# Kernel tuning notes

Measured on AMD Instinct MI355X. Metric: run time of the kernel, lower is better.

## Reference

```python
import jax, jax.numpy as jnp
import numpy as np

B, L, D_IN, D_MODEL, D_STATE, N_LAYERS = 16, 2048, 64, 512, 16, 4
LN_EPS = 1e-5


def setup_inputs() -> dict:
    key = jax.random.key(0)
    ks = jax.random.split(key, 16)
    s = 0.02
    x = jax.random.normal(ks[0], (B, L, D_IN), jnp.float32)
    W_in0 = jax.random.normal(ks[1], (D_IN, D_MODEL), jnp.float32) * s
    b_in0 = jnp.zeros((D_MODEL,), jnp.float32)
    W_in = jax.random.normal(ks[2], (N_LAYERS - 1, D_MODEL, D_MODEL), jnp.float32) * s
    b_in = jnp.zeros((N_LAYERS - 1, D_MODEL), jnp.float32)
    # S4D-style init: A_log = log(1..N) per channel
    A_log = jnp.broadcast_to(jnp.log(jnp.arange(1, D_STATE + 1, dtype=jnp.float32)), (N_LAYERS, D_MODEL, D_STATE)).copy()
    D_skip = jnp.ones((N_LAYERS, D_MODEL), jnp.float32)
    W_dt = jax.random.normal(ks[3], (N_LAYERS, D_MODEL, D_MODEL), jnp.float32) * s
    b_dt = jnp.full((N_LAYERS, D_MODEL), -4.0, jnp.float32)  # small initial dt
    W_B = jax.random.normal(ks[4], (N_LAYERS, D_MODEL, D_STATE), jnp.float32) * s
    W_C = jax.random.normal(ks[5], (N_LAYERS, D_MODEL, D_STATE), jnp.float32) * s
    ln_g = jnp.ones((D_MODEL,), jnp.float32)
    ln_b = jnp.zeros((D_MODEL,), jnp.float32)
    head_w = jax.random.normal(ks[6], (D_MODEL, 1), jnp.float32) * s
    head_b = jnp.zeros((1,), jnp.float32)
    return {"x": x, "W_in0": W_in0, "b_in0": b_in0, "W_in": W_in, "b_in": b_in,
            "A_log": A_log, "D_skip": D_skip, "W_dt": W_dt, "b_dt": b_dt,
            "W_B": W_B, "W_C": W_C, "ln_g": ln_g, "ln_b": ln_b,
            "head_w": head_w, "head_b": head_b}


def _mamba_layer(x, W_in_l, b_in_l, A_log_l, D_l, W_dt_l, b_dt_l, W_B_l, W_C_l):
    # x: (B, L, d_in) -> y: (B, L, D_MODEL)
    u = x @ W_in_l + b_in_l                    # (B, L, D)
    dt = jax.nn.softplus(u @ W_dt_l + b_dt_l)  # (B, L, D)
    Bm = u @ W_B_l                             # (B, L, N)
    Cm = u @ W_C_l                             # (B, L, N)
    A = -jnp.exp(A_log_l)                      # (D, N)

    def step(h, inp):
        dt_t, u_t, B_t, C_t = inp              # (B,D),(B,D),(B,N),(B,N)
        dA = jnp.exp(dt_t[..., None] * A)      # (B, D, N)
        h = dA * h + (dt_t * u_t)[..., None] * B_t[:, None, :]
        y_t = jnp.einsum('bdn,bn->bd', h, C_t)
        return h, y_t

    h0 = jnp.zeros((u.shape[0], u.shape[2], A.shape[1]), u.dtype)
    xs = (jnp.swapaxes(dt, 0, 1), jnp.swapaxes(u, 0, 1),
          jnp.swapaxes(Bm, 0, 1), jnp.swapaxes(Cm, 0, 1))
    _, ys = jax.lax.scan(step, h0, xs)         # ys: (L, B, D)
    return jnp.swapaxes(ys, 0, 1) + u * D_l


def reference(x, W_in0, b_in0, W_in, b_in, A_log, D_skip, W_dt, b_dt, W_B, W_C, ln_g, ln_b, head_w, head_b):
    h = x
    for i in range(N_LAYERS):
        Wi = W_in0 if i == 0 else W_in[i - 1]
        bi = b_in0 if i == 0 else b_in[i - 1]
        h = _mamba_layer(h, Wi, bi, A_log[i], D_skip[i], W_dt[i], b_dt[i], W_B[i], W_C[i])
    # LayerNorm over d_model
    mu = jnp.mean(h, axis=-1, keepdims=True)
    var = jnp.mean(jnp.square(h - mu), axis=-1, keepdims=True)
    h = (h - mu) * jax.lax.rsqrt(var + LN_EPS) * ln_g + ln_b
    return h[:, -1, :] @ head_w + head_b       # (B, 1)
```

## Files before the change

### kernel.cpp

```cpp
#include <hip/hip_runtime.h>
#include <hip/hip_bf16.h>
#include <cstdint>
#include <cstddef>

#define B_SZ    16
#define L_SZ    2048
#define DIN     64
#define DMODEL  512
#define DSTATE  16
#define NLAYERS 4
#define LN_EPS  1e-5f
#define NC      32
#define TCH     (L_SZ / NC)
#define NFUSED  (2 * DMODEL)

typedef __bf16 bf16x8 __attribute__((ext_vector_type(8)));
typedef float  f32x4  __attribute__((ext_vector_type(4)));
typedef unsigned short u16;
typedef unsigned int   u32;

__device__ __forceinline__ u16 f2bf(float f) {
    u32 u = __builtin_bit_cast(u32, f);
    u += 0x7fffu + ((u >> 16) & 1u);
    return (u16)(u >> 16);
}
__device__ __forceinline__ float bf2f(u16 v) {
    u32 u = ((u32)v) << 16;
    return __builtin_bit_cast(float, u);
}

__device__ __forceinline__ void pow16(float q, float* a_) {
    float q2 = q * q, q4 = q2 * q2, q8 = q4 * q4;
    a_[0] = q;        a_[1] = q2;       a_[2] = q2 * q;   a_[3] = q4;
    a_[4] = q4 * q;   a_[5] = q4 * q2;  a_[6] = a_[5] * q; a_[7] = q8;
    a_[8] = q8 * q;   a_[9] = q8 * q2;  a_[10] = a_[9] * q; a_[11] = q8 * q4;
    a_[12] = a_[11] * q; a_[13] = a_[11] * q2; a_[14] = a_[13] * q; a_[15] = q8 * q8;
}

#define LOG2E 1.4426950408889634f

__device__ __forceinline__ void gload16(const void* g, void* l) {
    __builtin_amdgcn_global_load_lds(
        (__attribute__((address_space(1))) void*)(g),
        (__attribute__((address_space(3))) void*)(l), 16, 0, 0);
}

template <int K>
__global__ __launch_bounds__(512) void gemm_fused(
    const u16* __restrict__ A, const u16* __restrict__ BT,
    const float* __restrict__ bias, u16* __restrict__ Cu,
    u16* __restrict__ Cdt, int M)
{
    constexpr int BM = 128, BK = 64;
    constexpr int NT = K / BK;
    __shared__ u16 As[2][BM * BK];
    __shared__ u16 Bs[2][BM * BK];

    const int tid = threadIdx.x;
    const int wv = tid >> 6, ln = tid & 63;
    const int mb = blockIdx.x & 255, nb = blockIdx.x >> 8;
    const int bm = mb * BM, bn = nb * BM;
    const int wm = (wv >> 1) * 32, wn = (wv & 1) * 64;

    f32x4 acc[2][4];
#pragma unroll
    for (int i = 0; i < 2; ++i)
#pragma unroll
        for (int j = 0; j < 4; ++j) acc[i][j] = (f32x4){0.f, 0.f, 0.f, 0.f};

    auto stage = [&](int buf, int k0) {
#pragma unroll
        for (int i = 0; i < 2; ++i) {
            int t = i * 512 + tid;
            int m = t >> 3, s = t & 7;
            int ksrc = (s ^ (m & 7)) * 8;
            gload16(A + (size_t)(bm + m) * K + k0 + ksrc,
                    &As[buf][(i * 512 + wv * 64) * 8]);
            gload16(BT + (size_t)(bn + m) * K + k0 + ksrc,
                    &Bs[buf][(i * 512 + wv * 64) * 8]);
        }
    };

    stage(0, 0);
    if (NT > 1) stage(1, BK);

#pragma unroll
    for (int kt = 0; kt < NT; ++kt) {
        if (kt == NT - 1) asm volatile("s_waitcnt vmcnt(0)" ::: "memory");
        else              asm volatile("s_waitcnt vmcnt(4)" ::: "memory");
        __builtin_amdgcn_s_barrier();

        const int buf = kt & 1;
#pragma unroll
        for (int ks = 0; ks < 2; ++ks) {
            bf16x8 af[2], bfr[4];
            const int g = ln >> 4, lm = ln & 15;
            const int c = ks * 4 + g;
#pragma unroll
            for (int e = 0; e < 2; ++e) {
                int ml = wm + e * 16 + lm;
                af[e] = *(const bf16x8*)&As[buf][ml * 64 + ((c ^ (ml & 7)) * 8)];
            }
#pragma unroll
            for (int f = 0; f < 4; ++f) {
                int nl = wn + f * 16 + lm;
                bfr[f] = *(const bf16x8*)&Bs[buf][nl * 64 + ((c ^ (nl & 7)) * 8)];
            }
#pragma unroll
            for (int e = 0; e < 2; ++e)
#pragma unroll
                for (int f = 0; f < 4; ++f)
                    acc[e][f] = __builtin_amdgcn_mfma_f32_16x16x32_bf16(
                        af[e], bfr[f], acc[e][f], 0, 0, 0);
        }

        asm volatile("s_waitcnt lgkmcnt(0)" ::: "memory");
        __builtin_amdgcn_s_barrier();
        if (kt + 2 < NT) stage(buf, (kt + 2) * BK);
    }

    const int cg = ln >> 4, lc = ln & 15;
    const bool uside = (bn < DMODEL);
#pragma unroll
    for (int e = 0; e < 2; ++e) {
#pragma unroll
        for (int f = 0; f < 4; ++f) {
            int col = bn + wn + f * 16 + lc;
            float bv = bias[col];
#pragma unroll
            for (int r = 0; r < 4; ++r) {
                int row = bm + wm + e * 16 + cg * 4 + r;
                float v = acc[e][f][r] + bv;
                if (uside) {
                    Cu[(size_t)row * DMODEL + col] = f2bf(v);
                } else {
                    v = (v > 20.f) ? v : __logf(1.f + __expf(v));
                    Cdt[(size_t)row * DMODEL + (col - DMODEL)] = f2bf(v);
                }
            }
        }
    }
}

__global__ __launch_bounds__(256) void wtrans(
    const float* __restrict__ W, u16* __restrict__ WT, int K, int N,
    size_t inStride, size_t outStride)
{
    __shared__ float tile[32][33];
    const float* Wm = W + (size_t)blockIdx.z * inStride;
    u16* WTm = WT + (size_t)blockIdx.z * outStride;
    int k0 = blockIdx.x * 32, n0 = blockIdx.y * 32;
    int tx = threadIdx.x & 31, ty = threadIdx.x >> 5;
#pragma unroll
    for (int i = 0; i < 4; ++i)
        tile[ty + 8 * i][tx] = Wm[(size_t)(k0 + ty + 8 * i) * N + n0 + tx];
    __syncthreads();
#pragma unroll
    for (int i = 0; i < 4; ++i)
        WTm[(size_t)(n0 + ty + 8 * i) * K + k0 + tx] = f2bf(tile[tx][ty + 8 * i]);
}

__global__ __launch_bounds__(256) void wcombo(
    const float* __restrict__ Win, const float* __restrict__ Wdt,
    u16* __restrict__ outT, int KD,
    size_t winStride, size_t wdtStride, size_t outStride)
{
    __shared__ float wi[16][516];
    __shared__ float wd[512][16];
    const float* WinL = Win + (size_t)blockIdx.z * winStride;
    const float* WdtL = Wdt + (size_t)blockIdx.z * wdtStride;
    u16* outL = outT + (size_t)blockIdx.z * outStride;
    const int k0 = blockIdx.x * 16, n0 = blockIdx.y * 16;
    const int tid = threadIdx.x;
    for (int i = tid; i < 16 * 128; i += 256) {
        int r = i >> 7, c = i & 127;
        *(float4*)&wi[r][c * 4] =
            *(const float4*)&WinL[(size_t)(k0 + r) * DMODEL + c * 4];
    }
    for (int i = tid; i < 512 * 4; i += 256) {
        int j = i >> 2, c = i & 3;
        *(float4*)&wd[j][c * 4] =
            *(const float4*)&WdtL[(size_t)j * DMODEL + n0 + c * 4];
    }
    __syncthreads();
    const int kk = tid & 15, nn = tid >> 4;
    float acc = 0.f;
#pragma unroll 8
    for (int j = 0; j < 512; ++j)
        acc = fmaf(wi[kk][j], wd[j][nn], acc);
    outL[(size_t)(n0 + nn) * KD + k0 + kk] = f2bf(acc);
}

__global__ __launch_bounds__(256) void biasprep(
    const float* __restrict__ bin, const float* __restrict__ Wdt,
    const float* __restrict__ bdt, float* __restrict__ biascat,
    size_t binStride, size_t wdtStride, size_t bdtStride, size_t outStride)
{
    const float* binL = bin + (size_t)blockIdx.z * binStride;
    const float* WdtL = Wdt + (size_t)blockIdx.z * wdtStride;
    const float* bdtL = bdt + (size_t)blockIdx.z * bdtStride;
    float* outL = biascat + (size_t)blockIdx.z * outStride;
    int idx = blockIdx.x * 256 + threadIdx.x;
    if (idx < DMODEL) { outL[idx] = binL[idx]; return; }
    int n = idx - DMODEL;
    float acc = bdtL[n];
    for (int j = 0; j < DMODEL; ++j)
        acc = fmaf(binL[j], WdtL[(size_t)j * DMODEL + n], acc);
    outL[idx] = acc;
}

__global__ __launch_bounds__(256) void castx(
    const float* __restrict__ x, u16* __restrict__ xb, int n4)
{
    int i = blockIdx.x * 256 + threadIdx.x;
    if (i < n4) {
        float4 v = ((const float4*)x)[i];
        ushort4 o;
        o.x = f2bf(v.x); o.y = f2bf(v.y); o.z = f2bf(v.z); o.w = f2bf(v.w);
        ((ushort4*)xb)[i] = o;
    }
}

__global__ __launch_bounds__(256) void prep_wbc(
    const float* __restrict__ WB, const float* __restrict__ WC,
    u16* __restrict__ WBCT)
{
    int idx = blockIdx.x * 256 + threadIdx.x;
    int l = idx >> 14;
    int r = idx & 16383;
    int n = r >> 9, k = r & 511;
    float v = (n < 16) ? WB[((size_t)l * DMODEL + k) * DSTATE + n]
                       : WC[((size_t)l * DMODEL + k) * DSTATE + (n - 16)];
    WBCT[((size_t)l * 32 + n) * DMODEL + k] = f2bf(v);
}

__global__ __launch_bounds__(256) void gemm_bc_mfma(
    const u16* __restrict__ A, const u16* __restrict__ WBCT,
    float* __restrict__ Bo, float* __restrict__ Co)
{
    const int tid = threadIdx.x;
    const int wv = tid >> 6, ln = tid & 63;
    const int m0 = blockIdx.x * 64 + wv * 16;
    const int g = ln >> 4, lm = ln & 15;

    f32x4 accB = (f32x4){0.f, 0.f, 0.f, 0.f};
    f32x4 accC = (f32x4){0.f, 0.f, 0.f, 0.f};
    const u16* arow = A + (size_t)(m0 + lm) * DMODEL;
    const u16* wb = WBCT + (size_t)lm * DMODEL;
    const u16* wc = WBCT + (size_t)(lm + 16) * DMODEL;
#pragma unroll
    for (int ks = 0; ks < DMODEL / 32; ++ks) {
        int ko = ks * 32 + g * 8;
        bf16x8 a = *(const bf16x8*)&arow[ko];
        bf16x8 b = *(const bf16x8*)&wb[ko];
        bf16x8 c = *(const bf16x8*)&wc[ko];
        accB = __builtin_amdgcn_mfma_f32_16x16x32_bf16(a, b, accB, 0, 0, 0);
        accC = __builtin_amdgcn_mfma_f32_16x16x32_bf16(a, c, accC, 0, 0, 0);
    }
#pragma unroll
    for (int r = 0; r < 4; ++r) {
        int m = m0 + g * 4 + r;
        Bo[(size_t)m * DSTATE + lm] = accB[r];
        Co[(size_t)m * DSTATE + lm] = accC[r];
    }
}

__global__ __launch_bounds__(256) void scan_pass1(
    const u16* __restrict__ u, const u16* __restrict__ dt,
    const float* __restrict__ Bm, const float* __restrict__ A_log,
    float* __restrict__ P, float* __restrict__ S)
{
    const int tid = threadIdx.x;
    const int d = blockIdx.x * 256 + tid;
    const int c = blockIdx.y, b = blockIdx.z;
    __shared__ float Bs[TCH][DSTATE];

    const float* Bsrc = Bm + ((size_t)b * L_SZ + (size_t)c * TCH) * DSTATE;
    for (int i = tid; i < TCH * DSTATE / 4; i += 256)
        ((float4*)Bs)[i] = ((const float4*)Bsrc)[i];

    float Ac[16];
#pragma unroll
    for (int n = 0; n < 16; ++n) Ac[n] = -__expf(A_log[d * DSTATE + n]);
    bool geo = true;
#pragma unroll
    for (int n = 1; n < 16; ++n)
        geo &= fabsf(Ac[n] - (n + 1) * Ac[0]) <= 1e-4f * (n + 1) * fabsf(Ac[0]);
    __syncthreads();

    float s[16];
#pragma unroll
    for (int n = 0; n < 16; ++n) s[n] = 0.f;

    const size_t base = ((size_t)b * L_SZ + (size_t)c * TCH) * DMODEL + d;
    size_t o = (((size_t)b * NC + c) * DMODEL + d) * DSTATE;

    if (geo) {
        const float cK = Ac[0] * LOG2E;
        float qp = 1.f;
#pragma unroll 2
        for (int t = 0; t < TCH; ++t) {
            float dtv = bf2f(dt[base + (size_t)t * DMODEL]);
            float uv  = bf2f(u [base + (size_t)t * DMODEL]);
            float du = dtv * uv;
            float q = exp2f(dtv * cK);
            qp *= q;
            float a_[16];
            pow16(q, a_);
#pragma unroll
            for (int n = 0; n < 16; ++n)
                s[n] = fmaf(a_[n], s[n], du * Bs[t][n]);
        }
        float p_[16];
        pow16(qp, p_);
#pragma unroll
        for (int n = 0; n < 16; ++n) { P[o + n] = p_[n]; S[o + n] = s[n]; }
    } else {
        float p[16];
#pragma unroll
        for (int n = 0; n < 16; ++n) p[n] = 1.f;
#pragma unroll 2
        for (int t = 0; t < TCH; ++t) {
            float dtv = bf2f(dt[base + (size_t)t * DMODEL]);
            float uv  = bf2f(u [base + (size_t)t * DMODEL]);
            float du = dtv * uv;
#pragma unroll
            for (int n = 0; n < 16; ++n) {
                float a = __expf(dtv * Ac[n]);
                p[n] *= a;
                s[n] = fmaf(a, s[n], du * Bs[t][n]);
            }
        }
#pragma unroll
        for (int n = 0; n < 16; ++n) { P[o + n] = p[n]; S[o + n] = s[n]; }
    }
}

__global__ __launch_bounds__(256) void scan_fix(
    const float* __restrict__ P, const float* __restrict__ S,
    float* __restrict__ H0)
{
    const int idx = blockIdx.x * 256 + threadIdx.x;
    const int dn = idx & (DMODEL * DSTATE - 1);
    const int b = idx >> 13;
    float h = 0.f;
#pragma unroll
    for (int c = 0; c < NC; ++c) {
        size_t o = (((size_t)b * NC + c) << 13) + dn;
        H0[o] = h;
        h = fmaf(P[o], h, S[o]);
    }
}

__global__ __launch_bounds__(256) void scan_pass2(
    const u16* __restrict__ u, const u16* __restrict__ dt,
    const float* __restrict__ Bm, const float* __restrict__ Cm,
    const float* __restrict__ A_log, const float* __restrict__ Dskip,
    const float* __restrict__ H0, u16* __restrict__ yb,
    float* __restrict__ ylast)
{
    const int tid = threadIdx.x;
    const int d = blockIdx.x * 256 + tid;
    const int c = blockIdx.y, b = blockIdx.z;
    __shared__ float Bs[TCH][DSTATE];
    __shared__ float Cs[TCH][DSTATE];

    const float* Bsrc = Bm + ((size_t)b * L_SZ + (size_t)c * TCH) * DSTATE;
    const float* Csrc = Cm + ((size_t)b * L_SZ + (size_t)c * TCH) * DSTATE;
    for (int i = tid; i < TCH * DSTATE / 4; i += 256) {
        ((float4*)Bs)[i] = ((const float4*)Bsrc)[i];
        ((float4*)Cs)[i] = ((const float4*)Csrc)[i];
    }

    float Ac[16];
#pragma unroll
    for (int n = 0; n < 16; ++n) Ac[n] = -__expf(A_log[d * DSTATE + n]);
    bool geo = true;
#pragma unroll
    for (int n = 1; n < 16; ++n)
        geo &= fabsf(Ac[n] - (n + 1) * Ac[0]) <= 1e-4f * (n + 1) * fabsf(Ac[0]);
    const float Dk = Dskip[d];

    float h[16];
    size_t ho = (((size_t)b * NC + c) * DMODEL + d) * DSTATE;
#pragma unroll
    for (int n = 0; n < 16; ++n) h[n] = H0[ho + n];
    __syncthreads();

    const size_t base = ((size_t)b * L_SZ + (size_t)c * TCH) * DMODEL + d;

    if (geo) {
        const float cK = Ac[0] * LOG2E;
#pragma unroll 2
        for (int t = 0; t < TCH; ++t) {
            float dtv = bf2f(dt[base + (size_t)t * DMODEL]);
            float uv  = bf2f(u [base + (size_t)t * DMODEL]);
            float du = dtv * uv;
            float q = exp2f(dtv * cK);
            float a_[16];
            pow16(q, a_);
            float yv = 0.f;
#pragma unroll
            for (int n = 0; n < 16; ++n) {
                h[n] = fmaf(a_[n], h[n], du * Bs[t][n]);
                yv = fmaf(h[n], Cs[t][n], yv);
            }
            yv = fmaf(uv, Dk, yv);
            yb[base + (size_t)t * DMODEL] = f2bf(yv);
            if (c == NC - 1 && t == TCH - 1) ylast[(size_t)b * DMODEL + d] = yv;
        }
    } else {
#pragma unroll 2
        for (int t = 0; t < TCH; ++t) {
            float dtv = bf2f(dt[base + (size_t)t * DMODEL]);
            float uv  = bf2f(u [base + (size_t)t * DMODEL]);
            float du = dtv * uv;
            float yv = 0.f;
#pragma unroll
            for (int n = 0; n < 16; ++n) {
                float a = __expf(dtv * Ac[n]);
                h[n] = fmaf(a, h[n], du * Bs[t][n]);
                yv = fmaf(h[n], Cs[t][n], yv);
            }
            yv = fmaf(uv, Dk, yv);
            yb[base + (size_t)t * DMODEL] = f2bf(yv);
            if (c == NC - 1 && t == TCH - 1) ylast[(size_t)b * DMODEL + d] = yv;
        }
    }
}

__global__ __launch_bounds__(256) void ln_head_kernel(
    const float* __restrict__ ylast, const float* __restrict__ g,
    const float* __restrict__ bb, const float* __restrict__ hw,
    const float* __restrict__ hb, float* __restrict__ out)
{
    const int b = blockIdx.x;
    const int tid = threadIdx.x;
    const float* row = ylast + (size_t)b * DMODEL;
    float v0 = row[tid], v1 = row[tid + 256];
    float s = v0 + v1;
    float s2 = v0 * v0 + v1 * v1;
#pragma unroll
    for (int o = 32; o >= 1; o >>= 1) {
        s += __shfl_xor(s, o);
        s2 += __shfl_xor(s2, o);
    }
    __shared__ float red[8];
    const int w = tid >> 6;
    if ((tid & 63) == 0) { red[w] = s; red[4 + w] = s2; }
    __syncthreads();
    s = red[0] + red[1] + red[2] + red[3];
    s2 = red[4] + red[5] + red[6] + red[7];
    float mu = s * (1.f / DMODEL);
    float var = s2 * (1.f / DMODEL) - mu * mu;
    float r = rsqrtf(var + LN_EPS);
    float c = ((v0 - mu) * r * g[tid] + bb[tid]) * hw[tid]
            + ((v1 - mu) * r * g[tid + 256] + bb[tid + 256]) * hw[tid + 256];
#pragma unroll
    for (int o = 32; o >= 1; o >>= 1) c += __shfl_xor(c, o);
    __syncthreads();
    if ((tid & 63) == 0) red[w] = c;
    __syncthreads();
    if (tid == 0) out[b] = red[0] + red[1] + red[2] + red[3] + hb[0];
}

extern "C" void kernel_launch(void* const* d_in, const int* in_sizes, int n_in,
                              void* d_out, int out_size, void* d_ws, size_t ws_size,
                              hipStream_t stream)
{
    const float* x      = (const float*)d_in[0];
    const float* W_in0  = (const float*)d_in[1];
    const float* b_in0  = (const float*)d_in[2];
    const float* W_in   = (const float*)d_in[3];
    const float* b_in   = (const float*)d_in[4];
    const float* A_log  = (const float*)d_in[5];
    const float* D_skip = (const float*)d_in[6];
    const float* W_dt   = (const float*)d_in[7];
    const float* b_dt   = (const float*)d_in[8];
    const float* W_B    = (const float*)d_in[9];
    const float* W_C    = (const float*)d_in[10];
    const float* ln_g   = (const float*)d_in[11];
    const float* ln_b   = (const float*)d_in[12];
    const float* head_w = (const float*)d_in[13];
    const float* head_b = (const float*)d_in[14];
    float* out = (float*)d_out;

    const size_t BLD = (size_t)B_SZ * L_SZ * DMODEL;
    const size_t BLN = (size_t)B_SZ * L_SZ * DSTATE;
    const size_t BCD = (size_t)B_SZ * NC * DMODEL * DSTATE;
    const size_t XBN = (size_t)B_SZ * L_SZ * DIN;

    float* fp = (float*)d_ws;
    float* Bbuf  = fp; fp += BLN;
    float* Cbuf  = fp; fp += BLN;
    float* Pbuf  = fp; fp += BCD;
    float* Sbuf  = fp; fp += BCD;
    float* H0buf = fp; fp += BCD;
    float* ylast = fp; fp += (size_t)B_SZ * DMODEL;
    float* biascat = fp; fp += (size_t)NLAYERS * NFUSED;
    u16* hp = (u16*)fp;
    u16* xb    = hp; hp += XBN;
    u16* ub    = hp; hp += BLD;
    u16* dtb   = hp; hp += BLD;
    u16* ybuf  = hp; hp += BLD;
    u16* BT0   = hp; hp += (size_t)NFUSED * DIN;
    u16* BTcat = hp; hp += (size_t)(NLAYERS - 1) * NFUSED * DMODEL;
    u16* WBCT  = hp; hp += (size_t)NLAYERS * 32 * DMODEL;

    const int M = B_SZ * L_SZ;

    castx<<<(XBN / 4 + 255) / 256, 256, 0, stream>>>(x, xb, XBN / 4);
    prep_wbc<<<(NLAYERS * 32 * DMODEL) / 256, 256, 0, stream>>>(W_B, W_C, WBCT);
    wtrans<<<dim3(DIN / 32, DMODEL / 32, 1), 256, 0, stream>>>(
        W_in0, BT0, DIN, DMODEL, 0, 0);
    wcombo<<<dim3(DIN / 16, DMODEL / 16, 1), 256, 0, stream>>>(
        W_in0, W_dt, BT0 + (size_t)DMODEL * DIN, DIN, 0, 0, 0);
    biasprep<<<dim3(4, 1, 1), 256, 0, stream>>>(
        b_in0, W_dt, b_dt, biascat, 0, 0, 0, 0);
    wtrans<<<dim3(DMODEL / 32, DMODEL / 32, NLAYERS - 1), 256, 0, stream>>>(
        W_in, BTcat, DMODEL, DMODEL,
        (size_t)DMODEL * DMODEL, (size_t)NFUSED * DMODEL);
    wcombo<<<dim3(DMODEL / 16, DMODEL / 16, NLAYERS - 1), 256, 0, stream>>>(
        W_in, W_dt + (size_t)DMODEL * DMODEL,
        BTcat + (size_t)DMODEL * DMODEL, DMODEL,
        (size_t)DMODEL * DMODEL, (size_t)DMODEL * DMODEL,
        (size_t)NFUSED * DMODEL);
    biasprep<<<dim3(4, 1, NLAYERS - 1), 256, 0, stream>>>(
        b_in, W_dt + (size_t)DMODEL * DMODEL, b_dt + DMODEL, biascat + NFUSED,
        DMODEL, (size_t)DMODEL * DMODEL, DMODEL, NFUSED);

    for (int l = 0; l < NLAYERS; ++l) {
        if (l == 0) {
            gemm_fused<DIN><<<(M / 128) * (NFUSED / 128), 512, 0, stream>>>(
                xb, BT0, biascat, ub, dtb, M);
        } else {
            gemm_fused<DMODEL><<<(M / 128) * (NFUSED / 128), 512, 0, stream>>>(
                ybuf, BTcat + (size_t)(l - 1) * NFUSED * DMODEL,
                biascat + (size_t)l * NFUSED, ub, dtb, M);
        }
        gemm_bc_mfma<<<M / 64, 256, 0, stream>>>(
            ub, WBCT + (size_t)l * 32 * DMODEL, Bbuf, Cbuf);
        const float* Al = A_log + (size_t)l * DMODEL * DSTATE;
        scan_pass1<<<dim3(DMODEL / 256, NC, B_SZ), 256, 0, stream>>>(
            ub, dtb, Bbuf, Al, Pbuf, Sbuf);
        scan_fix<<<(B_SZ * DMODEL * DSTATE) / 256, 256, 0, stream>>>(
            Pbuf, Sbuf, H0buf);
        scan_pass2<<<dim3(DMODEL / 256, NC, B_SZ), 256, 0, stream>>>(
            ub, dtb, Bbuf, Cbuf, Al, D_skip + (size_t)l * DMODEL,
            H0buf, ybuf, ylast);
    }

    ln_head_kernel<<<B_SZ, 256, 0, stream>>>(ylast, ln_g, ln_b, head_w, head_b, out);
}
```

Measured before the change: 700.8 us.

## Fold B/C projections into fused GEMM via precomposed weights; store chunk decay base

Precomposes W_in·W_B and W_in·W_C into extra columns of the fused input GEMM (padded to 1152 columns), so B and C come out of the same GEMM and the separate gemm_bc_mfma launch and its extra read of u are removed. The MFMA operand order is swapped so each lane holds four consecutive columns, which allows vectorised ushort4/float4 epilogue stores. Scan pass1 now writes a single per-channel decay base Q instead of 16 powers P, and scan_fix rebuilds the powers by repeated squaring when A is detected to be geometric. In exchange, one 128-column tile is wasted on 32 useful columns, a memset of the weight buffers is added, and B/C now come from bf16 composed weights, which changes the rounding.

```diff
diff --git a/kernel.cpp b/kernel.cpp
--- a/kernel.cpp
+++ b/kernel.cpp
@@ -12,7 +12,7 @@
 #define LN_EPS  1e-5f
 #define NC      32
 #define TCH     (L_SZ / NC)
-#define NFUSED  (2 * DMODEL)
+#define NFULL   1152
 
 typedef __bf16 bf16x8 __attribute__((ext_vector_type(8)));
 typedef float  f32x4  __attribute__((ext_vector_type(4)));
@@ -49,7 +49,8 @@
 __global__ __launch_bounds__(512) void gemm_fused(
     const u16* __restrict__ A, const u16* __restrict__ BT,
     const float* __restrict__ bias, u16* __restrict__ Cu,
-    u16* __restrict__ Cdt, int M)
+    u16* __restrict__ Cdt, float* __restrict__ Bo, float* __restrict__ Co,
+    int M)
 {
     constexpr int BM = 128, BK = 64;
     constexpr int NT = K / BK;
@@ -111,7 +112,7 @@
 #pragma unroll
                 for (int f = 0; f < 4; ++f)
                     acc[e][f] = __builtin_amdgcn_mfma_f32_16x16x32_bf16(
-                        af[e], bfr[f], acc[e][f], 0, 0, 0);
+                        bfr[f], af[e], acc[e][f], 0, 0, 0);
         }
 
         asm volatile("s_waitcnt lgkmcnt(0)" ::: "memory");
@@ -119,23 +120,45 @@
         if (kt + 2 < NT) stage(buf, (kt + 2) * BK);
     }
 
-    const int cg = ln >> 4, lc = ln & 15;
-    const bool uside = (bn < DMODEL);
+    const int cg = ln >> 4, lm = ln & 15;
 #pragma unroll
     for (int e = 0; e < 2; ++e) {
+        const int rowm = bm + wm + e * 16 + lm;
 #pragma unroll
         for (int f = 0; f < 4; ++f) {
-            int col = bn + wn + f * 16 + lc;
-            float bv = bias[col];
-#pragma unroll
-            for (int r = 0; r < 4; ++r) {
-                int row = bm + wm + e * 16 + cg * 4 + r;
-                float v = acc[e][f][r] + bv;
-                if (uside) {
-                    Cu[(size_t)row * DMODEL + col] = f2bf(v);
-                } else {
-                    v = (v > 20.f) ? v : __logf(1.f + __expf(v));
-                    Cdt[(size_t)row * DMODEL + (col - DMODEL)] = f2bf(v);
+            const int nc0 = bn + wn + f * 16 + cg * 4;
+            if (bn < DMODEL) {
+                float4 bv = *(const float4*)&bias[nc0];
+                ushort4 o;
+                o.x = f2bf(acc[e][f][0] + bv.x);
+                o.y = f2bf(acc[e][f][1] + bv.y);
+                o.z = f2bf(acc[e][f][2] + bv.z);
+                o.w = f2bf(acc[e][f][3] + bv.w);
+                *(ushort4*)&Cu[(size_t)rowm * DMODEL + nc0] = o;
+            } else if (bn < 2 * DMODEL) {
+                float4 bv = *(const float4*)&bias[nc0];
+                float v0 = acc[e][f][0] + bv.x, v1 = acc[e][f][1] + bv.y;
+                float v2 = acc[e][f][2] + bv.z, v3 = acc[e][f][3] + bv.w;
+                v0 = (v0 > 20.f) ? v0 : __logf(1.f + __expf(v0));
+                v1 = (v1 > 20.f) ? v1 : __logf(1.f + __expf(v1));
+                v2 = (v2 > 20.f) ? v2 : __logf(1.f + __expf(v2));
+                v3 = (v3 > 20.f) ? v3 : __logf(1.f + __expf(v3));
+                ushort4 o;
+                o.x = f2bf(v0); o.y = f2bf(v1); o.z = f2bf(v2); o.w = f2bf(v3);
+                *(ushort4*)&Cdt[(size_t)rowm * DMODEL + (nc0 - DMODEL)] = o;
+            } else {
+                if (nc0 < 2 * DMODEL + DSTATE) {
+                    float4 bv = *(const float4*)&bias[nc0];
+                    float4 o;
+                    o.x = acc[e][f][0] + bv.x; o.y = acc[e][f][1] + bv.y;
+                    o.z = acc[e][f][2] + bv.z; o.w = acc[e][f][3] + bv.w;
+                    *(float4*)&Bo[(size_t)rowm * DSTATE + (nc0 - 2 * DMODEL)] = o;
+                } else if (nc0 < 2 * DMODEL + 2 * DSTATE) {
+                    float4 bv = *(const float4*)&bias[nc0];
+                    float4 o;
+                    o.x = acc[e][f][0] + bv.x; o.y = acc[e][f][1] + bv.y;
+                    o.z = acc[e][f][2] + bv.z; o.w = acc[e][f][3] + bv.w;
+                    *(float4*)&Co[(size_t)rowm * DSTATE + (nc0 - 2 * DMODEL - DSTATE)] = o;
                 }
             }
         }
@@ -161,14 +184,14 @@
 }
 
 __global__ __launch_bounds__(256) void wcombo(
-    const float* __restrict__ Win, const float* __restrict__ Wdt,
-    u16* __restrict__ outT, int KD,
-    size_t winStride, size_t wdtStride, size_t outStride)
+    const float* __restrict__ Win, const float* __restrict__ Wr,
+    u16* __restrict__ outT, int KD, int wrRow,
+    size_t winStride, size_t wrStride, size_t outStride)
 {
     __shared__ float wi[16][516];
     __shared__ float wd[512][16];
     const float* WinL = Win + (size_t)blockIdx.z * winStride;
-    const float* WdtL = Wdt + (size_t)blockIdx.z * wdtStride;
+    const float* WrL  = Wr  + (size_t)blockIdx.z * wrStride;
     u16* outL = outT + (size_t)blockIdx.z * outStride;
     const int k0 = blockIdx.x * 16, n0 = blockIdx.y * 16;
     const int tid = threadIdx.x;
@@ -180,7 +203,7 @@
     for (int i = tid; i < 512 * 4; i += 256) {
         int j = i >> 2, c = i & 3;
         *(float4*)&wd[j][c * 4] =
-            *(const float4*)&WdtL[(size_t)j * DMODEL + n0 + c * 4];
+            *(const float4*)&WrL[(size_t)j * wrRow + n0 + c * 4];
     }
     __syncthreads();
     const int kk = tid & 15, nn = tid >> 4;
@@ -193,20 +216,41 @@
 
 __global__ __launch_bounds__(256) void biasprep(
     const float* __restrict__ bin, const float* __restrict__ Wdt,
+    const float* __restrict__ WB, const float* __restrict__ WC,
     const float* __restrict__ bdt, float* __restrict__ biascat,
-    size_t binStride, size_t wdtStride, size_t bdtStride, size_t outStride)
+    size_t binStride, size_t wdtStride, size_t wbcStride,
+    size_t bdtStride, size_t outStride)
 {
     const float* binL = bin + (size_t)blockIdx.z * binStride;
     const float* WdtL = Wdt + (size_t)blockIdx.z * wdtStride;
+    const float* WBL  = WB  + (size_t)blockIdx.z * wbcStride;
+    const float* WCL  = WC  + (size_t)blockIdx.z * wbcStride;
     const float* bdtL = bdt + (size_t)blockIdx.z * bdtStride;
     float* outL = biascat + (size_t)blockIdx.z * outStride;
     int idx = blockIdx.x * 256 + threadIdx.x;
-    if (idx < DMODEL) { outL[idx] = binL[idx]; return; }
-    int n = idx - DMODEL;
-    float acc = bdtL[n];
-    for (int j = 0; j < DMODEL; ++j)
-        acc = fmaf(binL[j], WdtL[(size_t)j * DMODEL + n], acc);
-    outL[idx] = acc;
+    if (idx >= NFULL) return;
+    float v;
+    if (idx < DMODEL) {
+        v = binL[idx];
+    } else if (idx < 2 * DMODEL) {
+        int n = idx - DMODEL;
+        v = bdtL[n];
+        for (int j = 0; j < DMODEL; ++j)
+            v = fmaf(binL[j], WdtL[(size_t)j * DMODEL + n], v);
+    } else if (idx < 2 * DMODEL + DSTATE) {
+        int n = idx - 2 * DMODEL;
+        v = 0.f;
+        for (int j = 0; j < DMODEL; ++j)
+            v = fmaf(binL[j], WBL[(size_t)j * DSTATE + n], v);
+    } else if (idx < 2 * DMODEL + 2 * DSTATE) {
+        int n = idx - 2 * DMODEL - DSTATE;
+        v = 0.f;
+        for (int j = 0; j < DMODEL; ++j)
+            v = fmaf(binL[j], WCL[(size_t)j * DSTATE + n], v);
+    } else {
+        v = 0.f;
+    }
+    outL[idx] = v;
 }
 
 __global__ __launch_bounds__(256) void castx(
@@ -221,54 +265,10 @@
     }
 }
 
-__global__ __launch_bounds__(256) void prep_wbc(
-    const float* __restrict__ WB, const float* __restrict__ WC,
-    u16* __restrict__ WBCT)
-{
-    int idx = blockIdx.x * 256 + threadIdx.x;
-    int l = idx >> 14;
-    int r = idx & 16383;
-    int n = r >> 9, k = r & 511;
-    float v = (n < 16) ? WB[((size_t)l * DMODEL + k) * DSTATE + n]
-                       : WC[((size_t)l * DMODEL + k) * DSTATE + (n - 16)];
-    WBCT[((size_t)l * 32 + n) * DMODEL + k] = f2bf(v);
-}
-
-__global__ __launch_bounds__(256) void gemm_bc_mfma(
-    const u16* __restrict__ A, const u16* __restrict__ WBCT,
-    float* __restrict__ Bo, float* __restrict__ Co)
-{
-    const int tid = threadIdx.x;
-    const int wv = tid >> 6, ln = tid & 63;
-    const int m0 = blockIdx.x * 64 + wv * 16;
-    const int g = ln >> 4, lm = ln & 15;
-
-    f32x4 accB = (f32x4){0.f, 0.f, 0.f, 0.f};
-    f32x4 accC = (f32x4){0.f, 0.f, 0.f, 0.f};
-    const u16* arow = A + (size_t)(m0 + lm) * DMODEL;
-    const u16* wb = WBCT + (size_t)lm * DMODEL;
-    const u16* wc = WBCT + (size_t)(lm + 16) * DMODEL;
-#pragma unroll
-    for (int ks = 0; ks < DMODEL / 32; ++ks) {
-        int ko = ks * 32 + g * 8;
-        bf16x8 a = *(const bf16x8*)&arow[ko];
-        bf16x8 b = *(const bf16x8*)&wb[ko];
-        bf16x8 c = *(const bf16x8*)&wc[ko];
-        accB = __builtin_amdgcn_mfma_f32_16x16x32_bf16(a, b, accB, 0, 0, 0);
-        accC = __builtin_amdgcn_mfma_f32_16x16x32_bf16(a, c, accC, 0, 0, 0);
-    }
-#pragma unroll
-    for (int r = 0; r < 4; ++r) {
-        int m = m0 + g * 4 + r;
-        Bo[(size_t)m * DSTATE + lm] = accB[r];
-        Co[(size_t)m * DSTATE + lm] = accC[r];
-    }
-}
-
 __global__ __launch_bounds__(256) void scan_pass1(
     const u16* __restrict__ u, const u16* __restrict__ dt,
     const float* __restrict__ Bm, const float* __restrict__ A_log,
-    float* __restrict__ P, float* __restrict__ S)
+    float* __restrict__ P, float* __restrict__ S, float* __restrict__ Q)
 {
     const int tid = threadIdx.x;
     const int d = blockIdx.x * 256 + tid;
@@ -311,10 +311,9 @@
             for (int n = 0; n < 16; ++n)
                 s[n] = fmaf(a_[n], s[n], du * Bs[t][n]);
         }
-        float p_[16];
-        pow16(qp, p_);
-#pragma unroll
-        for (int n = 0; n < 16; ++n) { P[o + n] = p_[n]; S[o + n] = s[n]; }
+        Q[((size_t)b * NC + c) * DMODEL + d] = qp;
+#pragma unroll
+        for (int n = 0; n < 16; ++n) S[o + n] = s[n];
     } else {
         float p[16];
 #pragma unroll
@@ -338,17 +337,42 @@
 
 __global__ __launch_bounds__(256) void scan_fix(
     const float* __restrict__ P, const float* __restrict__ S,
+    const float* __restrict__ Q, const float* __restrict__ A_log,
     float* __restrict__ H0)
 {
     const int idx = blockIdx.x * 256 + threadIdx.x;
     const int dn = idx & (DMODEL * DSTATE - 1);
     const int b = idx >> 13;
+    const int d = dn >> 4, n = dn & 15;
+
+    float Ac0 = -__expf(A_log[d * DSTATE + 0]);
+    bool geo = true;
+#pragma unroll
+    for (int j = 1; j < 16; ++j) {
+        float Acj = -__expf(A_log[d * DSTATE + j]);
+        geo &= fabsf(Acj - (j + 1) * Ac0) <= 1e-4f * (j + 1) * fabsf(Ac0);
+    }
+
     float h = 0.f;
 #pragma unroll
     for (int c = 0; c < NC; ++c) {
         size_t o = (((size_t)b * NC + c) << 13) + dn;
         H0[o] = h;
-        h = fmaf(P[o], h, S[o]);
+        float p;
+        if (geo) {
+            float base = Q[((size_t)b * NC + c) * DMODEL + d];
+            p = 1.f;
+            int e = n + 1;
+#pragma unroll
+            for (int i = 0; i < 5; ++i) {
+                if (e & 1) p *= base;
+                base *= base;
+                e >>= 1;
+            }
+        } else {
+            p = P[o];
+        }
+        h = fmaf(p, h, S[o]);
     }
 }
 
@@ -488,6 +512,7 @@
     const size_t BLD = (size_t)B_SZ * L_SZ * DMODEL;
     const size_t BLN = (size_t)B_SZ * L_SZ * DSTATE;
     const size_t BCD = (size_t)B_SZ * NC * DMODEL * DSTATE;
+    const size_t BCDQ = (size_t)B_SZ * NC * DMODEL;
     const size_t XBN = (size_t)B_SZ * L_SZ * DIN;
 
     float* fp = (float*)d_ws;
@@ -496,55 +521,64 @@
     float* Pbuf  = fp; fp += BCD;
     float* Sbuf  = fp; fp += BCD;
     float* H0buf = fp; fp += BCD;
+    float* Qbuf  = fp; fp += BCDQ;
     float* ylast = fp; fp += (size_t)B_SZ * DMODEL;
-    float* biascat = fp; fp += (size_t)NLAYERS * NFUSED;
+    float* biascat = fp; fp += (size_t)NLAYERS * NFULL;
     u16* hp = (u16*)fp;
     u16* xb    = hp; hp += XBN;
     u16* ub    = hp; hp += BLD;
     u16* dtb   = hp; hp += BLD;
     u16* ybuf  = hp; hp += BLD;
-    u16* BT0   = hp; hp += (size_t)NFUSED * DIN;
-    u16* BTcat = hp; hp += (size_t)(NLAYERS - 1) * NFUSED * DMODEL;
-    u16* WBCT  = hp; hp += (size_t)NLAYERS * 32 * DMODEL;
+    u16* BT0   = hp; hp += (size_t)NFULL * DIN;
+    u16* BTcat = hp; hp += (size_t)(NLAYERS - 1) * NFULL * DMODEL;
 
     const int M = B_SZ * L_SZ;
-
+    const size_t WDM = (size_t)DMODEL * DMODEL;
+    const size_t WBN = (size_t)DMODEL * DSTATE;
+
+    hipMemsetAsync(BT0, 0,
+        ((size_t)NFULL * DIN + (size_t)(NLAYERS - 1) * NFULL * DMODEL) * sizeof(u16),
+        stream);
     castx<<<(XBN / 4 + 255) / 256, 256, 0, stream>>>(x, xb, XBN / 4);
-    prep_wbc<<<(NLAYERS * 32 * DMODEL) / 256, 256, 0, stream>>>(W_B, W_C, WBCT);
     wtrans<<<dim3(DIN / 32, DMODEL / 32, 1), 256, 0, stream>>>(
         W_in0, BT0, DIN, DMODEL, 0, 0);
     wcombo<<<dim3(DIN / 16, DMODEL / 16, 1), 256, 0, stream>>>(
-        W_in0, W_dt, BT0 + (size_t)DMODEL * DIN, DIN, 0, 0, 0);
-    biasprep<<<dim3(4, 1, 1), 256, 0, stream>>>(
-        b_in0, W_dt, b_dt, biascat, 0, 0, 0, 0);
+        W_in0, W_dt, BT0 + (size_t)DMODEL * DIN, DIN, DMODEL, 0, 0, 0);
+    wcombo<<<dim3(DIN / 16, 1, 1), 256, 0, stream>>>(
+        W_in0, W_B, BT0 + (size_t)2 * DMODEL * DIN, DIN, DSTATE, 0, 0, 0);
+    wcombo<<<dim3(DIN / 16, 1, 1), 256, 0, stream>>>(
+        W_in0, W_C, BT0 + ((size_t)2 * DMODEL + DSTATE) * DIN, DIN, DSTATE, 0, 0, 0);
+    biasprep<<<dim3(5, 1, 1), 256, 0, stream>>>(
+        b_in0, W_dt, W_B, W_C, b_dt, biascat, 0, 0, 0, 0, 0);
     wtrans<<<dim3(DMODEL / 32, DMODEL / 32, NLAYERS - 1), 256, 0, stream>>>(
-        W_in, BTcat, DMODEL, DMODEL,
-        (size_t)DMODEL * DMODEL, (size_t)NFUSED * DMODEL);
+        W_in, BTcat, DMODEL, DMODEL, WDM, (size_t)NFULL * DMODEL);
     wcombo<<<dim3(DMODEL / 16, DMODEL / 16, NLAYERS - 1), 256, 0, stream>>>(
-        W_in, W_dt + (size_t)DMODEL * DMODEL,
-        BTcat + (size_t)DMODEL * DMODEL, DMODEL,
-        (size_t)DMODEL * DMODEL, (size_t)DMODEL * DMODEL,
-        (size_t)NFUSED * DMODEL);
-    biasprep<<<dim3(4, 1, NLAYERS - 1), 256, 0, stream>>>(
-        b_in, W_dt + (size_t)DMODEL * DMODEL, b_dt + DMODEL, biascat + NFUSED,
-        DMODEL, (size_t)DMODEL * DMODEL, DMODEL, NFUSED);
+        W_in, W_dt + WDM, BTcat + (size_t)DMODEL * DMODEL, DMODEL, DMODEL,
+        WDM, WDM, (size_t)NFULL * DMODEL);
+    wcombo<<<dim3(DMODEL / 16, 1, NLAYERS - 1), 256, 0, stream>>>(
+        W_in, W_B + WBN, BTcat + (size_t)2 * DMODEL * DMODEL, DMODEL, DSTATE,
+        WDM, WBN, (size_t)NFULL * DMODEL);
+    wcombo<<<dim3(DMODEL / 16, 1, NLAYERS - 1), 256, 0, stream>>>(
+        W_in, W_C + WBN, BTcat + ((size_t)2 * DMODEL + DSTATE) * DMODEL, DMODEL,
+        DSTATE, WDM, WBN, (size_t)NFULL * DMODEL);
+    biasprep<<<dim3(5, 1, NLAYERS - 1), 256, 0, stream>>>(
+        b_in, W_dt + WDM, W_B + WBN, W_C + WBN, b_dt + DMODEL, biascat + NFULL,
+        DMODEL, WDM, WBN, DMODEL, NFULL);
 
     for (int l = 0; l < NLAYERS; ++l) {
         if (l == 0) {
-            gemm_fused<DIN><<<(M / 128) * (NFUSED / 128), 512, 0, stream>>>(
-                xb, BT0, biascat, ub, dtb, M);
+            gemm_fused<DIN><<<(M / 128) * (NFULL / 128), 512, 0, stream>>>(
+                xb, BT0, biascat, ub, dtb, Bbuf, Cbuf, M);
         } else {
-            gemm_fused<DMODEL><<<(M / 128) * (NFUSED / 128), 512, 0, stream>>>(
-                ybuf, BTcat + (size_t)(l - 1) * NFUSED * DMODEL,
-                biascat + (size_t)l * NFUSED, ub, dtb, M);
-        }
-        gemm_bc_mfma<<<M / 64, 256, 0, stream>>>(
-            ub, WBCT + (size_t)l * 32 * DMODEL, Bbuf, Cbuf);
+            gemm_fused<DMODEL><<<(M / 128) * (NFULL / 128), 512, 0, stream>>>(
+                ybuf, BTcat + (size_t)(l - 1) * NFULL * DMODEL,
+                biascat + (size_t)l * NFULL, ub, dtb, Bbuf, Cbuf, M);
+        }
         const float* Al = A_log + (size_t)l * DMODEL * DSTATE;
         scan_pass1<<<dim3(DMODEL / 256, NC, B_SZ), 256, 0, stream>>>(
-            ub, dtb, Bbuf, Al, Pbuf, Sbuf);
+            ub, dtb, Bbuf, Al, Pbuf, Sbuf, Qbuf);
         scan_fix<<<(B_SZ * DMODEL * DSTATE) / 256, 256, 0, stream>>>(
-            Pbuf, Sbuf, H0buf);
+            Pbuf, Sbuf, Qbuf, Al, H0buf);
         scan_pass2<<<dim3(DMODEL / 256, NC, B_SZ), 256, 0, stream>>>(
             ub, dtb, Bbuf, Cbuf, Al, D_skip + (size_t)l * DMODEL,
             H0buf, ybuf, ylast);
```

After: 764.7 us. 9.1% more time.

## Stage u/dt chunks in LDS and store scalar chunk decay instead of per-state P

Applied to the files above, without the earlier changes.

Both scan passes now preload the block's u and dt chunk into shared memory with 16-byte vector loads, replacing strided 2-byte per-thread global loads inside the time loop. For the geometric-A case, pass1 writes a single cumulative decay per (b,c,d) instead of 16 P values, and scan_fix rebuilds the powers from it. This cuts P traffic and write bandwidth at the cost of extra LDS (about 64KB per block) that may lower occupancy, plus redundant A_log geometry checks in scan_fix.

```diff
diff --git a/kernel.cpp b/kernel.cpp
--- a/kernel.cpp
+++ b/kernel.cpp
@@ -268,17 +268,31 @@
 __global__ __launch_bounds__(256) void scan_pass1(
     const u16* __restrict__ u, const u16* __restrict__ dt,
     const float* __restrict__ Bm, const float* __restrict__ A_log,
-    float* __restrict__ P, float* __restrict__ S)
+    float* __restrict__ P, float* __restrict__ S, float* __restrict__ Q)
 {
     const int tid = threadIdx.x;
     const int d = blockIdx.x * 256 + tid;
     const int c = blockIdx.y, b = blockIdx.z;
     __shared__ float Bs[TCH][DSTATE];
+    __shared__ u16 Us[TCH][256];
+    __shared__ u16 Ds[TCH][256];
 
     const float* Bsrc = Bm + ((size_t)b * L_SZ + (size_t)c * TCH) * DSTATE;
     for (int i = tid; i < TCH * DSTATE / 4; i += 256)
         ((float4*)Bs)[i] = ((const float4*)Bsrc)[i];
 
+    const size_t base0 = ((size_t)b * L_SZ + (size_t)c * TCH) * DMODEL
+                       + (size_t)blockIdx.x * 256;
+#pragma unroll
+    for (int i = 0; i < 8; ++i) {
+        int idx = i * 256 + tid;
+        int t = idx >> 5, q = idx & 31;
+        *(uint4*)&Us[t][q * 8] =
+            *(const uint4*)&u[base0 + (size_t)t * DMODEL + q * 8];
+        *(uint4*)&Ds[t][q * 8] =
+            *(const uint4*)&dt[base0 + (size_t)t * DMODEL + q * 8];
+    }
+
     float Ac[16];
 #pragma unroll
     for (int n = 0; n < 16; ++n) Ac[n] = -__expf(A_log[d * DSTATE + n]);
@@ -292,7 +306,6 @@
 #pragma unroll
     for (int n = 0; n < 16; ++n) s[n] = 0.f;
 
-    const size_t base = ((size_t)b * L_SZ + (size_t)c * TCH) * DMODEL + d;
     size_t o = (((size_t)b * NC + c) * DMODEL + d) * DSTATE;
 
     if (geo) {
@@ -300,8 +313,8 @@
         float qp = 1.f;
 #pragma unroll 2
         for (int t = 0; t < TCH; ++t) {
-            float dtv = bf2f(dt[base + (size_t)t * DMODEL]);
-            float uv  = bf2f(u [base + (size_t)t * DMODEL]);
+            float dtv = bf2f(Ds[t][tid]);
+            float uv  = bf2f(Us[t][tid]);
             float du = dtv * uv;
             float q = exp2f(dtv * cK);
             qp *= q;
@@ -311,18 +324,17 @@
             for (int n = 0; n < 16; ++n)
                 s[n] = fmaf(a_[n], s[n], du * Bs[t][n]);
         }
-        float p_[16];
-        pow16(qp, p_);
-#pragma unroll
-        for (int n = 0; n < 16; ++n) { P[o + n] = p_[n]; S[o + n] = s[n]; }
+        Q[((size_t)b * NC + c) * DMODEL + d] = qp;
+#pragma unroll
+        for (int n = 0; n < 16; ++n) S[o + n] = s[n];
     } else {
         float p[16];
 #pragma unroll
         for (int n = 0; n < 16; ++n) p[n] = 1.f;
 #pragma unroll 2
         for (int t = 0; t < TCH; ++t) {
-            float dtv = bf2f(dt[base + (size_t)t * DMODEL]);
-            float uv  = bf2f(u [base + (size_t)t * DMODEL]);
+            float dtv = bf2f(Ds[t][tid]);
+            float uv  = bf2f(Us[t][tid]);
             float du = dtv * uv;
 #pragma unroll
             for (int n = 0; n < 16; ++n) {
@@ -338,17 +350,42 @@
 
 __global__ __launch_bounds__(256) void scan_fix(
     const float* __restrict__ P, const float* __restrict__ S,
+    const float* __restrict__ Q, const float* __restrict__ A_log,
     float* __restrict__ H0)
 {
     const int idx = blockIdx.x * 256 + threadIdx.x;
     const int dn = idx & (DMODEL * DSTATE - 1);
     const int b = idx >> 13;
+    const int d = dn >> 4, n = dn & 15;
+
+    float Ac0 = -__expf(A_log[d * DSTATE + 0]);
+    bool geo = true;
+#pragma unroll
+    for (int j = 1; j < 16; ++j) {
+        float Acj = -__expf(A_log[d * DSTATE + j]);
+        geo &= fabsf(Acj - (j + 1) * Ac0) <= 1e-4f * (j + 1) * fabsf(Ac0);
+    }
+
     float h = 0.f;
 #pragma unroll
     for (int c = 0; c < NC; ++c) {
         size_t o = (((size_t)b * NC + c) << 13) + dn;
         H0[o] = h;
-        h = fmaf(P[o], h, S[o]);
+        float p;
+        if (geo) {
+            float base = Q[((size_t)b * NC + c) * DMODEL + d];
+            p = 1.f;
+            int e = n + 1;
+#pragma unroll
+            for (int i = 0; i < 5; ++i) {
+                if (e & 1) p *= base;
+                base *= base;
+                e >>= 1;
+            }
+        } else {
+            p = P[o];
+        }
+        h = fmaf(p, h, S[o]);
     }
 }
 
@@ -364,6 +401,8 @@
     const int c = blockIdx.y, b = blockIdx.z;
     __shared__ float Bs[TCH][DSTATE];
     __shared__ float Cs[TCH][DSTATE];
+    __shared__ u16 Us[TCH][256];
+    __shared__ u16 Ds[TCH][256];
 
     const float* Bsrc = Bm + ((size_t)b * L_SZ + (size_t)c * TCH) * DSTATE;
     const float* Csrc = Cm + ((size_t)b * L_SZ + (size_t)c * TCH) * DSTATE;
@@ -372,6 +411,18 @@
         ((float4*)Cs)[i] = ((const float4*)Csrc)[i];
     }
 
+    const size_t base0 = ((size_t)b * L_SZ + (size_t)c * TCH) * DMODEL
+                       + (size_t)blockIdx.x * 256;
+#pragma unroll
+    for (int i = 0; i < 8; ++i) {
+        int idx = i * 256 + tid;
+        int t = idx >> 5, q = idx & 31;
+        *(uint4*)&Us[t][q * 8] =
+            *(const uint4*)&u[base0 + (size_t)t * DMODEL + q * 8];
+        *(uint4*)&Ds[t][q * 8] =
+            *(const uint4*)&dt[base0 + (size_t)t * DMODEL + q * 8];
+    }
+
     float Ac[16];
 #pragma unroll
     for (int n = 0; n < 16; ++n) Ac[n] = -__expf(A_log[d * DSTATE + n]);
@@ -387,14 +438,14 @@
     for (int n = 0; n < 16; ++n) h[n] = H0[ho + n];
     __syncthreads();
 
-    const size_t base = ((size_t)b * L_SZ + (size_t)c * TCH) * DMODEL + d;
+    const size_t base = base0 - (size_t)blockIdx.x * 256 + d;
 
     if (geo) {
         const float cK = Ac[0] * LOG2E;
 #pragma unroll 2
         for (int t = 0; t < TCH; ++t) {
-            float dtv = bf2f(dt[base + (size_t)t * DMODEL]);
-            float uv  = bf2f(u [base + (size_t)t * DMODEL]);
+            float dtv = bf2f(Ds[t][tid]);
+            float uv  = bf2f(Us[t][tid]);
             float du = dtv * uv;
             float q = exp2f(dtv * cK);
             float a_[16];
@@ -412,8 +463,8 @@
     } else {
 #pragma unroll 2
         for (int t = 0; t < TCH; ++t) {
-            float dtv = bf2f(dt[base + (size_t)t * DMODEL]);
-            float uv  = bf2f(u [base + (size_t)t * DMODEL]);
+            float dtv = bf2f(Ds[t][tid]);
+            float uv  = bf2f(Us[t][tid]);
             float du = dtv * uv;
             float yv = 0.f;
 #pragma unroll
@@ -488,6 +539,7 @@
     const size_t BLD = (size_t)B_SZ * L_SZ * DMODEL;
     const size_t BLN = (size_t)B_SZ * L_SZ * DSTATE;
     const size_t BCD = (size_t)B_SZ * NC * DMODEL * DSTATE;
+    const size_t BCDQ = (size_t)B_SZ * NC * DMODEL;
     const size_t XBN = (size_t)B_SZ * L_SZ * DIN;
 
     float* fp = (float*)d_ws;
@@ -496,6 +548,7 @@
     float* Pbuf  = fp; fp += BCD;
     float* Sbuf  = fp; fp += BCD;
     float* H0buf = fp; fp += BCD;
+    float* Qbuf  = fp; fp += BCDQ;
     float* ylast = fp; fp += (size_t)B_SZ * DMODEL;
     float* biascat = fp; fp += (size_t)NLAYERS * NFUSED;
     u16* hp = (u16*)fp;
@@ -542,9 +595,9 @@
             ub, WBCT + (size_t)l * 32 * DMODEL, Bbuf, Cbuf);
         const float* Al = A_log + (size_t)l * DMODEL * DSTATE;
         scan_pass1<<<dim3(DMODEL / 256, NC, B_SZ), 256, 0, stream>>>(
-            ub, dtb, Bbuf, Al, Pbuf, Sbuf);
+            ub, dtb, Bbuf, Al, Pbuf, Sbuf, Qbuf);
         scan_fix<<<(B_SZ * DMODEL * DSTATE) / 256, 256, 0, stream>>>(
-            Pbuf, Sbuf, H0buf);
+            Pbuf, Sbuf, Qbuf, Al, H0buf);
         scan_pass2<<<dim3(DMODEL / 256, NC, B_SZ), 256, 0, stream>>>(
             ub, dtb, Bbuf, Cbuf, Al, D_skip + (size_t)l * DMODEL,
             H0buf, ybuf, ylast);
```

Result: slower. 796.0 us (+13.6%).
